# Kernel tuning notes

Measured on AMD Instinct MI355X. Metric: run time of the kernel, lower is better.

Reference implementation:

```python
import jax, jax.numpy as jnp
import numpy as np

MEM = 128   # mem_dim
K = 4096    # number of object keys (each an array leaf list)
L = 128     # numbers per array
STATS_CAP = 100  # number_stats list capped at 100 entries


def setup_inputs() -> dict:
    key = jax.random.key(0)
    ks = jax.random.split(key, 13)
    s = 0.05
    return {
        "numbers": jax.random.normal(ks[0], (K, L), jnp.float32),
        "w_num": jax.random.normal(ks[1], (MEM,), jnp.float32) * s,
        "b_num": jax.random.normal(ks[2], (MEM,), jnp.float32) * s,
        "W_ih": jax.random.normal(ks[3], (4 * MEM, 2 * MEM), jnp.float32) * s,
        "W_hh": jax.random.normal(ks[4], (4 * MEM, MEM), jnp.float32) * s,
        "b_ih": jax.random.normal(ks[5], (4 * MEM,), jnp.float32) * s,
        "b_hh": jax.random.normal(ks[6], (4 * MEM,), jnp.float32) * s,
        "W_fh": jax.random.normal(ks[7], (MEM, MEM), jnp.float32) * s,
        "b_fh": jax.random.normal(ks[8], (MEM,), jnp.float32) * s,
        "W_iouh": jax.random.normal(ks[9], (3 * MEM, MEM), jnp.float32) * s,
        "b_iouh": jax.random.normal(ks[10], (3 * MEM,), jnp.float32) * s,
        "W_lout": jax.random.normal(ks[11], (MEM, MEM), jnp.float32) * s,
        "b_lout": jax.random.normal(ks[12], (MEM,), jnp.float32) * s,
    }


def _normalize_numbers(x_flat):
    # Replicates embed_number's running number_stats (tie_primitives -> one shared
    # '___default___' stats list, filled in traversal order, capped at 100 entries).
    # The k-th number is normalized by mean/std over the first min(k, 100) numbers
    # (including itself); std division only when len > 3 and std not ~0.
    n = x_flat.shape[0]
    k = jnp.arange(1, n + 1, dtype=jnp.float32)
    cs = jnp.cumsum(x_flat)
    css = jnp.cumsum(x_flat * x_flat)
    cap = jnp.minimum(k, float(STATS_CAP))
    cs_c = jnp.where(k <= STATS_CAP, cs, cs[STATS_CAP - 1])
    css_c = jnp.where(k <= STATS_CAP, css, css[STATS_CAP - 1])
    mean = cs_c / cap
    var = jnp.maximum(css_c / cap - mean * mean, 0.0)
    std = jnp.sqrt(var)
    # torch impl computes stats with numpy -> no gradient flows through them
    mean = jax.lax.stop_gradient(mean)
    std = jax.lax.stop_gradient(std)
    y = x_flat - mean
    use_std = (cap > 3.0) & (std > 1e-8)
    return jnp.where(use_std, y / jnp.where(use_std, std, 1.0), y)


def _forward(numbers, w_num, b_num, W_ih, W_hh, b_ih, b_hh,
             W_fh, b_fh, W_iouh, b_iouh, W_lout, b_lout):
    # --- embed_number: per-leaf (c=0, h = Linear(1, MEM)(norm_num)) ---
    x = _normalize_numbers(numbers.reshape(-1)).reshape(K, L)
    h_num = x[..., None] * w_num + b_num  # [K, L, MEM]

    # --- embed_array: LSTMCell over each array's children; input = cat([c_child, h_child]) ---
    # child_c is always 0 for number leaves.
    def step(carry, h_t):  # h_t: [K, MEM]
        c, h = carry
        xcat = jnp.concatenate([jnp.zeros_like(h_t), h_t], axis=-1)  # [K, 2*MEM]
        gates = xcat @ W_ih.T + b_ih + h @ W_hh.T + b_hh             # [K, 4*MEM]
        i, f, g, o = jnp.split(gates, 4, axis=-1)
        c2 = jax.nn.sigmoid(f) * c + jax.nn.sigmoid(i) * jnp.tanh(g)
        h2 = jax.nn.sigmoid(o) * jnp.tanh(c2)
        return (c2, h2), None

    z = jnp.zeros((K, MEM), numbers.dtype)
    (c_arr, h_arr), _ = jax.lax.scan(step, (z, z), jnp.swapaxes(h_num, 0, 1))
    # c_arr, h_arr: [K, MEM] final states per array child of the root object

    # --- embed_object (root): child-sum Tree-LSTM gating ---
    f_g = jax.nn.sigmoid(h_arr @ W_fh.T + b_fh)             # [K, MEM]
    fc_sum = jnp.sum(f_g * c_arr, axis=0, keepdims=True)    # [1, MEM]
    hs_bar = jnp.sum(h_arr, axis=0, keepdims=True)          # [1, MEM]
    iou = hs_bar @ W_iouh.T + b_iouh
    i, o, u = jnp.split(iou, 3, axis=-1)
    c = jax.nn.sigmoid(i) * jnp.tanh(u) + fc_sum
    h = jax.nn.sigmoid(o) * jnp.tanh(c)
    h_hat = h @ W_lout.T + b_lout
    return jnp.concatenate([c, h_hat], axis=1)  # [1, 2*MEM]


def reference(numbers, w_num, b_num, W_ih, W_hh, b_ih, b_hh,
              W_fh, b_fh, W_iouh, b_iouh, W_lout, b_lout):
    return _forward(numbers, w_num, b_num, W_ih, W_hh, b_ih, b_hh,
                    W_fh, b_fh, W_iouh, b_iouh, W_lout, b_lout)
```

## Files before the change

### kernel.cpp

```cpp
#include <hip/hip_runtime.h>
#include <math.h>

#define MEM 128
#define HSTR 136

typedef __bf16 bf16x8 __attribute__((ext_vector_type(8)));
typedef float  f32x4  __attribute__((ext_vector_type(4)));

__device__ __forceinline__ float fast_rcp(float x) { return __builtin_amdgcn_rcpf(x); }
__device__ __forceinline__ float fast_sigmoid(float x) {
    return fast_rcp(1.0f + __expf(-x));
}
__device__ __forceinline__ float fast_tanh(float x) {
    return 1.0f - 2.0f * fast_rcp(__expf(2.0f * x) + 1.0f);
}

__global__ void prep_kernel(const float* __restrict__ numbers,
                            const float* __restrict__ w_num,
                            const float* __restrict__ b_num,
                            const float* __restrict__ W_ih,
                            const float* __restrict__ b_ih,
                            const float* __restrict__ b_hh,
                            float* __restrict__ mean_lut, float* __restrict__ inv_lut,
                            float* __restrict__ Avec, float* __restrict__ Bvec) {
    __shared__ float sx[100];
    __shared__ float swn[128], sbn[128];
    int tid = threadIdx.x;
    if (tid < 100) sx[tid] = numbers[tid];
    if (tid < 128) { swn[tid] = w_num[tid]; sbn[tid] = b_num[tid]; }
    __syncthreads();
    if (tid < 100) {
        float s = 0.f, ss = 0.f;
        for (int j = 0; j <= tid; ++j) { float v = sx[j]; s += v; ss += v * v; }
        float cap  = (float)(tid + 1);
        float mean = s / cap;
        float var  = ss / cap - mean * mean;
        if (var < 0.f) var = 0.f;
        float sd = sqrtf(var);
        float inv = (cap > 3.0f && sd > 1e-8f) ? (1.0f / sd) : 1.0f;
        mean_lut[tid] = mean;
        inv_lut[tid]  = inv;
    }
    const int part  = tid & 3;
    const int jbase = tid >> 2;
    #pragma unroll
    for (int round = 0; round < 4; ++round) {
        int j = jbase + round * 128;
        const float* row = W_ih + j * 256 + 128 + part * 32;
        const float* wn  = swn + part * 32;
        const float* bn  = sbn + part * 32;
        float a = 0.f, b = 0.f;
        #pragma unroll
        for (int m = 0; m < 32; m += 4) {
            f32x4 w = *(const f32x4*)(row + m);
            a += w[0] * wn[m]     + w[1] * wn[m + 1] + w[2] * wn[m + 2] + w[3] * wn[m + 3];
            b += w[0] * bn[m]     + w[1] * bn[m + 1] + w[2] * bn[m + 2] + w[3] * bn[m + 3];
        }
        a += __shfl_xor(a, 1); a += __shfl_xor(a, 2);
        b += __shfl_xor(b, 1); b += __shfl_xor(b, 2);
        if (part == 0) { Avec[j] = a; Bvec[j] = b + b_ih[j] + b_hh[j]; }
    }
}

__global__ __launch_bounds__(512, 2) void lstm_kernel(
        const float* __restrict__ numbers, const float* __restrict__ W_hh,
        const float* __restrict__ W_fh,    const float* __restrict__ b_fh,
        const float* __restrict__ mean_lut, const float* __restrict__ inv_lut,
        const float* __restrict__ Avec,     const float* __restrict__ Bvec,
        float* __restrict__ fc_sum, float* __restrict__ hs_bar) {
    __shared__ unsigned short hbuf[2][16 * HSTR];
    __shared__ float xls[128 * 16];

    const int tid  = threadIdx.x;
    const int lane = tid & 63;
    const int wave = tid >> 6;
    const int quad = lane >> 4;
    const int lcol = lane & 15;
    const int m0   = wave * 16;
    const int r0   = blockIdx.x * 16;

    for (int i = tid; i < 16 * 128; i += 512) {
        int row = i >> 7;
        int t   = i & 127;
        int flat = (r0 + row) * 128 + t;
        int ii = (flat < 100) ? flat : 99;
        float v = numbers[flat];
        xls[t * 16 + row] = (v - mean_lut[ii]) * inv_lut[ii];
    }
    for (int i = tid; i < 16 * HSTR; i += 512) hbuf[0][i] = 0;

    bf16x8 bf[4][4];
    #pragma unroll
    for (int g = 0; g < 4; ++g) {
        #pragma unroll
        for (int kk = 0; kk < 4; ++kk) {
            int j = g * 128 + m0 + lcol;
            const float* p = W_hh + j * 128 + kk * 32 + quad * 8;
            f32x4 w0 = *(const f32x4*)p;
            f32x4 w1 = *(const f32x4*)(p + 4);
            bf16x8 bt;
            #pragma unroll
            for (int q = 0; q < 4; ++q) { bt[q] = (__bf16)w0[q]; bt[q + 4] = (__bf16)w1[q]; }
            bf[g][kk] = bt;
        }
    }
    float ag[4], bg[4];
    #pragma unroll
    for (int g = 0; g < 4; ++g) {
        ag[g] = Avec[g * 128 + m0 + lcol];
        bg[g] = Bvec[g * 128 + m0 + lcol];
    }

    float c[4]  = {0.f, 0.f, 0.f, 0.f};
    float hf[4] = {0.f, 0.f, 0.f, 0.f};
    __syncthreads();

    auto step = [&](int t, const unsigned short* hin, unsigned short* hout) {
        bf16x8 af[4];
        #pragma unroll
        for (int kk = 0; kk < 4; ++kk)
            af[kk] = *(const bf16x8*)(const void*)(hin + lcol * HSTR + kk * 32 + quad * 8);
        f32x4 xq = *(const f32x4*)(const void*)(xls + t * 16 + quad * 4);
        f32x4 acc[4];
        #pragma unroll
        for (int g = 0; g < 4; ++g) {
            f32x4 a0;
            #pragma unroll
            for (int r = 0; r < 4; ++r) a0[r] = xq[r] * ag[g] + bg[g];
            #pragma unroll
            for (int kk = 0; kk < 4; ++kk)
                a0 = __builtin_amdgcn_mfma_f32_16x16x32_bf16(af[kk], bf[g][kk], a0, 0, 0, 0);
            acc[g] = a0;
        }
        #pragma unroll
        for (int r = 0; r < 4; ++r) {
            float si = fast_sigmoid(acc[0][r]);
            float sf = fast_sigmoid(acc[1][r]);
            float tg = fast_tanh(acc[2][r]);
            float so = fast_sigmoid(acc[3][r]);
            float c2 = sf * c[r] + si * tg;
            c[r] = c2;
            float h = so * fast_tanh(c2);
            hf[r] = h;
            hout[(quad * 4 + r) * HSTR + m0 + lcol] = __builtin_bit_cast(unsigned short, (__bf16)h);
        }
        __syncthreads();
    };

    for (int t = 0; t < 128; t += 2) {
        step(t,     hbuf[0], hbuf[1]);
        step(t + 1, hbuf[1], hbuf[0]);
    }

    float v = hf[0] + hf[1] + hf[2] + hf[3];
    v += __shfl_xor(v, 16);
    v += __shfl_xor(v, 32);
    if (lane < 16) atomicAdd(&hs_bar[m0 + lane], v);

    f32x4 facc;
    {
        float bb = b_fh[m0 + lcol];
        #pragma unroll
        for (int r = 0; r < 4; ++r) facc[r] = bb;
    }
    #pragma unroll
    for (int kk = 0; kk < 4; ++kk) {
        bf16x8 afr = *(const bf16x8*)(const void*)(hbuf[0] + lcol * HSTR + kk * 32 + quad * 8);
        const float* p = W_fh + (m0 + lcol) * 128 + kk * 32 + quad * 8;
        f32x4 w0 = *(const f32x4*)p;
        f32x4 w1 = *(const f32x4*)(p + 4);
        bf16x8 wt;
        #pragma unroll
        for (int q = 0; q < 4; ++q) { wt[q] = (__bf16)w0[q]; wt[q + 4] = (__bf16)w1[q]; }
        facc = __builtin_amdgcn_mfma_f32_16x16x32_bf16(afr, wt, facc, 0, 0, 0);
    }
    float fcv = 0.f;
    #pragma unroll
    for (int r = 0; r < 4; ++r) fcv += fast_sigmoid(facc[r]) * c[r];
    fcv += __shfl_xor(fcv, 16);
    fcv += __shfl_xor(fcv, 32);
    if (lane < 16) atomicAdd(&fc_sum[m0 + lane], fcv);
}

__global__ void finalize_kernel(const float* __restrict__ fc_sum,
                                const float* __restrict__ hs_bar,
                                const float* __restrict__ W_iouh,
                                const float* __restrict__ b_iouh,
                                const float* __restrict__ W_lout,
                                const float* __restrict__ b_lout,
                                float* __restrict__ out) {
    __shared__ float hsb[128], iou[384], hfin[128];
    int tid = threadIdx.x;
    const int part = tid & 3;
    const int jb   = tid >> 2;
    if (tid < 128) hsb[tid] = hs_bar[tid];
    __syncthreads();
    #pragma unroll
    for (int round = 0; round < 3; ++round) {
        int j = jb + round * 128;
        const float* row = W_iouh + j * 128 + part * 32;
        const float* hv  = hsb + part * 32;
        float s = 0.f;
        #pragma unroll
        for (int m = 0; m < 32; m += 4) {
            f32x4 w = *(const f32x4*)(row + m);
            s += w[0] * hv[m] + w[1] * hv[m + 1] + w[2] * hv[m + 2] + w[3] * hv[m + 3];
        }
        s += __shfl_xor(s, 1); s += __shfl_xor(s, 2);
        if (part == 0) iou[j] = s + b_iouh[j];
    }
    __syncthreads();
    if (tid < 128) {
        float i = iou[tid], o = iou[128 + tid], u = iou[256 + tid];
        float cf = fast_sigmoid(i) * fast_tanh(u) + fc_sum[tid];
        out[tid] = cf;
        hfin[tid] = fast_sigmoid(o) * fast_tanh(cf);
    }
    __syncthreads();
    {
        const float* row = W_lout + jb * 128 + part * 32;
        const float* hv  = hfin + part * 32;
        float s = 0.f;
        #pragma unroll
        for (int m = 0; m < 32; m += 4) {
            f32x4 w = *(const f32x4*)(row + m);
            s += w[0] * hv[m] + w[1] * hv[m + 1] + w[2] * hv[m + 2] + w[3] * hv[m + 3];
        }
        s += __shfl_xor(s, 1); s += __shfl_xor(s, 2);
        if (part == 0) out[128 + jb] = s + b_lout[jb];
    }
}

extern "C" void kernel_launch(void* const* d_in, const int* in_sizes, int n_in,
                              void* d_out, int out_size, void* d_ws, size_t ws_size,
                              hipStream_t stream) {
    const float* numbers = (const float*)d_in[0];
    const float* w_num   = (const float*)d_in[1];
    const float* b_num   = (const float*)d_in[2];
    const float* W_ih    = (const float*)d_in[3];
    const float* W_hh    = (const float*)d_in[4];
    const float* b_ih    = (const float*)d_in[5];
    const float* b_hh    = (const float*)d_in[6];
    const float* W_fh    = (const float*)d_in[7];
    const float* b_fh    = (const float*)d_in[8];
    const float* W_iouh  = (const float*)d_in[9];
    const float* b_iouh  = (const float*)d_in[10];
    const float* W_lout  = (const float*)d_in[11];
    const float* b_lout  = (const float*)d_in[12];
    float* out = (float*)d_out;

    float* ws       = (float*)d_ws;
    float* fc_sum   = ws;
    float* hs_bar   = ws + 128;
    float* mean_lut = ws + 256;
    float* inv_lut  = ws + 356;
    float* Avec     = ws + 456;
    float* Bvec     = ws + 968;

    hipMemsetAsync(fc_sum, 0, 256 * sizeof(float), stream);
    prep_kernel<<<1, 512, 0, stream>>>(numbers, w_num, b_num, W_ih, b_ih, b_hh,
                                       mean_lut, inv_lut, Avec, Bvec);
    lstm_kernel<<<256, 512, 0, stream>>>(numbers, W_hh, W_fh, b_fh,
                                         mean_lut, inv_lut, Avec, Bvec, fc_sum, hs_bar);
    finalize_kernel<<<1, 512, 0, stream>>>(fc_sum, hs_bar, W_iouh, b_iouh, W_lout, b_lout, out);
}
```

Measured before the change: 215.3 us.

## Fuse prep, LSTM and finalize kernels into one launch with ticket-based tail

Result: slower. 237.3 us (+10.2%).

```diff
diff --git a/kernel.cpp b/kernel.cpp
--- a/kernel.cpp
+++ b/kernel.cpp
@@ -3,73 +3,35 @@
 
 #define MEM 128
 #define HSTR 136
+#define LOG2E 1.4426950408889634f
 
 typedef __bf16 bf16x8 __attribute__((ext_vector_type(8)));
 typedef float  f32x4  __attribute__((ext_vector_type(4)));
 
 __device__ __forceinline__ float fast_rcp(float x) { return __builtin_amdgcn_rcpf(x); }
+__device__ __forceinline__ float fast_exp2(float x) { return __builtin_amdgcn_exp2f(x); }
 __device__ __forceinline__ float fast_sigmoid(float x) {
-    return fast_rcp(1.0f + __expf(-x));
+    return fast_rcp(1.0f + fast_exp2(-LOG2E * x));
 }
 __device__ __forceinline__ float fast_tanh(float x) {
-    return 1.0f - 2.0f * fast_rcp(__expf(2.0f * x) + 1.0f);
-}
-
-__global__ void prep_kernel(const float* __restrict__ numbers,
-                            const float* __restrict__ w_num,
-                            const float* __restrict__ b_num,
-                            const float* __restrict__ W_ih,
-                            const float* __restrict__ b_ih,
-                            const float* __restrict__ b_hh,
-                            float* __restrict__ mean_lut, float* __restrict__ inv_lut,
-                            float* __restrict__ Avec, float* __restrict__ Bvec) {
-    __shared__ float sx[100];
-    __shared__ float swn[128], sbn[128];
-    int tid = threadIdx.x;
-    if (tid < 100) sx[tid] = numbers[tid];
-    if (tid < 128) { swn[tid] = w_num[tid]; sbn[tid] = b_num[tid]; }
-    __syncthreads();
-    if (tid < 100) {
-        float s = 0.f, ss = 0.f;
-        for (int j = 0; j <= tid; ++j) { float v = sx[j]; s += v; ss += v * v; }
-        float cap  = (float)(tid + 1);
-        float mean = s / cap;
-        float var  = ss / cap - mean * mean;
-        if (var < 0.f) var = 0.f;
-        float sd = sqrtf(var);
-        float inv = (cap > 3.0f && sd > 1e-8f) ? (1.0f / sd) : 1.0f;
-        mean_lut[tid] = mean;
-        inv_lut[tid]  = inv;
-    }
-    const int part  = tid & 3;
-    const int jbase = tid >> 2;
-    #pragma unroll
-    for (int round = 0; round < 4; ++round) {
-        int j = jbase + round * 128;
-        const float* row = W_ih + j * 256 + 128 + part * 32;
-        const float* wn  = swn + part * 32;
-        const float* bn  = sbn + part * 32;
-        float a = 0.f, b = 0.f;
-        #pragma unroll
-        for (int m = 0; m < 32; m += 4) {
-            f32x4 w = *(const f32x4*)(row + m);
-            a += w[0] * wn[m]     + w[1] * wn[m + 1] + w[2] * wn[m + 2] + w[3] * wn[m + 3];
-            b += w[0] * bn[m]     + w[1] * bn[m + 1] + w[2] * bn[m + 2] + w[3] * bn[m + 3];
-        }
-        a += __shfl_xor(a, 1); a += __shfl_xor(a, 2);
-        b += __shfl_xor(b, 1); b += __shfl_xor(b, 2);
-        if (part == 0) { Avec[j] = a; Bvec[j] = b + b_ih[j] + b_hh[j]; }
-    }
-}
-
-__global__ __launch_bounds__(512, 2) void lstm_kernel(
-        const float* __restrict__ numbers, const float* __restrict__ W_hh,
-        const float* __restrict__ W_fh,    const float* __restrict__ b_fh,
-        const float* __restrict__ mean_lut, const float* __restrict__ inv_lut,
-        const float* __restrict__ Avec,     const float* __restrict__ Bvec,
-        float* __restrict__ fc_sum, float* __restrict__ hs_bar) {
+    return 2.0f * fast_rcp(1.0f + fast_exp2(-2.0f * LOG2E * x)) - 1.0f;
+}
+
+__global__ __launch_bounds__(512, 2) void fused_kernel(
+        const float* __restrict__ numbers, const float* __restrict__ w_num,
+        const float* __restrict__ b_num,   const float* __restrict__ W_ih,
+        const float* __restrict__ W_hh,    const float* __restrict__ b_ih,
+        const float* __restrict__ b_hh,    const float* __restrict__ W_fh,
+        const float* __restrict__ b_fh,    const float* __restrict__ W_iouh,
+        const float* __restrict__ b_iouh,  const float* __restrict__ W_lout,
+        const float* __restrict__ b_lout,
+        float* __restrict__ fc_sum, float* __restrict__ hs_bar,
+        int* __restrict__ ticket, float* __restrict__ out) {
     __shared__ unsigned short hbuf[2][16 * HSTR];
     __shared__ float xls[128 * 16];
+    __shared__ float mean_l[100], inv_l[100];
+    __shared__ float abv[1024];
+    __shared__ int   s_last;
 
     const int tid  = threadIdx.x;
     const int lane = tid & 63;
@@ -79,15 +41,47 @@
     const int m0   = wave * 16;
     const int r0   = blockIdx.x * 16;
 
+    if (tid < 100) xls[tid] = numbers[tid];
+    __syncthreads();
+    if (tid < 100) {
+        float s = 0.f, ss = 0.f;
+        for (int j = 0; j <= tid; ++j) { float v = xls[j]; s += v; ss += v * v; }
+        float cap  = (float)(tid + 1);
+        float mean = s / cap;
+        float var  = ss / cap - mean * mean;
+        if (var < 0.f) var = 0.f;
+        float sd = sqrtf(var);
+        float inv = (cap > 3.0f && sd > 1e-8f) ? (1.0f / sd) : 1.0f;
+        mean_l[tid] = mean;
+        inv_l[tid]  = inv;
+    }
+    {
+        const float* row = W_ih + tid * 256 + 128;
+        float a = 0.f, b = 0.f;
+        #pragma unroll
+        for (int m = 0; m < 128; m += 4) {
+            f32x4 w  = *(const f32x4*)(row + m);
+            f32x4 wn = *(const f32x4*)(w_num + m);
+            f32x4 bn = *(const f32x4*)(b_num + m);
+            a += w[0] * wn[0] + w[1] * wn[1] + w[2] * wn[2] + w[3] * wn[3];
+            b += w[0] * bn[0] + w[1] * bn[1] + w[2] * bn[2] + w[3] * bn[3];
+        }
+        abv[tid]       = a;
+        abv[512 + tid] = b + b_ih[tid] + b_hh[tid];
+    }
+    __syncthreads();
+
     for (int i = tid; i < 16 * 128; i += 512) {
         int row = i >> 7;
         int t   = i & 127;
         int flat = (r0 + row) * 128 + t;
         int ii = (flat < 100) ? flat : 99;
         float v = numbers[flat];
-        xls[t * 16 + row] = (v - mean_lut[ii]) * inv_lut[ii];
+        xls[t * 16 + row] = (v - mean_l[ii]) * inv_l[ii];
     }
     for (int i = tid; i < 16 * HSTR; i += 512) hbuf[0][i] = 0;
+
+    const float GS[4] = { -LOG2E, -LOG2E, -2.0f * LOG2E, -LOG2E };
 
     bf16x8 bf[4][4];
     #pragma unroll
@@ -100,15 +94,18 @@
             f32x4 w1 = *(const f32x4*)(p + 4);
             bf16x8 bt;
             #pragma unroll
-            for (int q = 0; q < 4; ++q) { bt[q] = (__bf16)w0[q]; bt[q + 4] = (__bf16)w1[q]; }
+            for (int q = 0; q < 4; ++q) {
+                bt[q]     = (__bf16)(w0[q] * GS[g]);
+                bt[q + 4] = (__bf16)(w1[q] * GS[g]);
+            }
             bf[g][kk] = bt;
         }
     }
     float ag[4], bg[4];
     #pragma unroll
     for (int g = 0; g < 4; ++g) {
-        ag[g] = Avec[g * 128 + m0 + lcol];
-        bg[g] = Bvec[g * 128 + m0 + lcol];
+        ag[g] = abv[g * 128 + m0 + lcol]       * GS[g];
+        bg[g] = abv[512 + g * 128 + m0 + lcol] * GS[g];
     }
 
     float c[4]  = {0.f, 0.f, 0.f, 0.f};
@@ -134,13 +131,14 @@
         }
         #pragma unroll
         for (int r = 0; r < 4; ++r) {
-            float si = fast_sigmoid(acc[0][r]);
-            float sf = fast_sigmoid(acc[1][r]);
-            float tg = fast_tanh(acc[2][r]);
-            float so = fast_sigmoid(acc[3][r]);
-            float c2 = sf * c[r] + si * tg;
+            float si = fast_rcp(1.0f + fast_exp2(acc[0][r]));
+            float sf = fast_rcp(1.0f + fast_exp2(acc[1][r]));
+            float rg = fast_rcp(1.0f + fast_exp2(acc[2][r]));
+            float so = fast_rcp(1.0f + fast_exp2(acc[3][r]));
+            float c2 = sf * c[r] + si * (2.0f * rg - 1.0f);
             c[r] = c2;
-            float h = so * fast_tanh(c2);
+            float rc = fast_rcp(1.0f + fast_exp2(-2.0f * LOG2E * c2));
+            float h  = so * (2.0f * rc - 1.0f);
             hf[r] = h;
             hout[(quad * 4 + r) * HSTR + m0 + lcol] = __builtin_bit_cast(unsigned short, (__bf16)h);
         }
@@ -180,21 +178,24 @@
     fcv += __shfl_xor(fcv, 16);
     fcv += __shfl_xor(fcv, 32);
     if (lane < 16) atomicAdd(&fc_sum[m0 + lane], fcv);
-}
-
-__global__ void finalize_kernel(const float* __restrict__ fc_sum,
-                                const float* __restrict__ hs_bar,
-                                const float* __restrict__ W_iouh,
-                                const float* __restrict__ b_iouh,
-                                const float* __restrict__ W_lout,
-                                const float* __restrict__ b_lout,
-                                float* __restrict__ out) {
-    __shared__ float hsb[128], iou[384], hfin[128];
-    int tid = threadIdx.x;
+
+    __threadfence();
+    __syncthreads();
+    if (tid == 0) {
+        int old = atomicAdd(ticket, 1);
+        s_last = (old == (int)gridDim.x - 1) ? 1 : 0;
+    }
+    __syncthreads();
+    if (!s_last) return;
+
+    __threadfence();
+    float* hsb  = xls;
+    float* iou  = xls + 128;
+    float* hfin = xls + 512;
+    if (tid < 128) hsb[tid] = atomicAdd(&hs_bar[tid], 0.0f);
+    __syncthreads();
     const int part = tid & 3;
     const int jb   = tid >> 2;
-    if (tid < 128) hsb[tid] = hs_bar[tid];
-    __syncthreads();
     #pragma unroll
     for (int round = 0; round < 3; ++round) {
         int j = jb + round * 128;
@@ -211,8 +212,9 @@
     }
     __syncthreads();
     if (tid < 128) {
+        float fcr = atomicAdd(&fc_sum[tid], 0.0f);
         float i = iou[tid], o = iou[128 + tid], u = iou[256 + tid];
-        float cf = fast_sigmoid(i) * fast_tanh(u) + fc_sum[tid];
+        float cf = fast_sigmoid(i) * fast_tanh(u) + fcr;
         out[tid] = cf;
         hfin[tid] = fast_sigmoid(o) * fast_tanh(cf);
     }
@@ -249,18 +251,13 @@
     const float* b_lout  = (const float*)d_in[12];
     float* out = (float*)d_out;
 
-    float* ws       = (float*)d_ws;
-    float* fc_sum   = ws;
-    float* hs_bar   = ws + 128;
-    float* mean_lut = ws + 256;
-    float* inv_lut  = ws + 356;
-    float* Avec     = ws + 456;
-    float* Bvec     = ws + 968;
-
-    hipMemsetAsync(fc_sum, 0, 256 * sizeof(float), stream);
-    prep_kernel<<<1, 512, 0, stream>>>(numbers, w_num, b_num, W_ih, b_ih, b_hh,
-                                       mean_lut, inv_lut, Avec, Bvec);
-    lstm_kernel<<<256, 512, 0, stream>>>(numbers, W_hh, W_fh, b_fh,
-                                         mean_lut, inv_lut, Avec, Bvec, fc_sum, hs_bar);
-    finalize_kernel<<<1, 512, 0, stream>>>(fc_sum, hs_bar, W_iouh, b_iouh, W_lout, b_lout, out);
-}
+    float* ws     = (float*)d_ws;
+    float* fc_sum = ws;
+    float* hs_bar = ws + 128;
+    int*   ticket = (int*)(ws + 256);
+
+    hipMemsetAsync(ws, 0, 257 * sizeof(float), stream);
+    fused_kernel<<<256, 512, 0, stream>>>(numbers, w_num, b_num, W_ih, W_hh, b_ih, b_hh,
+                                          W_fh, b_fh, W_iouh, b_iouh, W_lout, b_lout,
+                                          fc_sum, hs_bar, ticket, out);
+}
```
